# Optimization experiments

Hardware: AMD Instinct MI355X
Metric: run time of the kernel (lower is better)

Reference implementation:

```python
import jax, jax.numpy as jnp
import numpy as np
from jax import lax

B, N, H, W, C = 8, 1024, 256, 256, 256
HID = 512
RATES = (1, 3, 9, 9, 3, 1)


def setup_inputs() -> dict:
    key = jax.random.key(0)
    ks = jax.random.split(key, 16)
    # vertices are (row, col) float coordinates inside the feature map
    vertices = jax.random.uniform(ks[0], (B, N, 2), jnp.float32) * jnp.array([H - 1, W - 1], jnp.float32)
    features = jax.random.normal(ks[1], (B, H, W, C), jnp.float32)
    inp = {"vertices": vertices, "features": features}
    # Conv1D stack params (haiku Conv1D: kernel [K, Cin, Cout], bias [Cout])
    cin = C
    for i in range(6):
        inp[f"w{i}"] = jax.random.normal(ks[2 + 2 * i], (3, cin, HID), jnp.float32) * 0.05
        inp[f"b{i}"] = jax.random.normal(ks[3 + 2 * i], (HID,), jnp.float32) * 0.05
        cin = HID
    # offset head: Conv1D(2, 1, with_bias=False); original zero-init, randomized here
    inp["w_off"] = jax.random.normal(ks[14], (1, HID, 2), jnp.float32) * 0.05
    return inp


def _conv1d(x, w, b, rate):
    # x: [B, N, Cin], w: [K, Cin, Cout] -> SAME-padded dilated conv over vertex axis
    y = lax.conv_general_dilated(x, w, window_strides=(1,), padding="SAME",
                                 rhs_dilation=(rate,),
                                 dimension_numbers=("NWC", "WIO", "NWC"))
    return y if b is None else y + b


def _sample_at_vertices(vertices, features):
    # bilinear interpolation, zero outside (map_coordinates order=1 mode='constant')
    Bb, Hh, Ww, Cc = features.shape
    y, x = vertices[..., 0], vertices[..., 1]  # [B, N]
    y0f, x0f = jnp.floor(y), jnp.floor(x)
    wy1, wx1 = y - y0f, x - x0f
    wy0, wx0 = 1.0 - wy1, 1.0 - wx1
    y0, x0 = y0f.astype(jnp.int32), x0f.astype(jnp.int32)
    flat = features.reshape(Bb, Hh * Ww, Cc)

    def gather(yi, xi, wgt):
        valid = (yi >= 0) & (yi < Hh) & (xi >= 0) & (xi < Ww)
        idx = jnp.clip(yi, 0, Hh - 1) * Ww + jnp.clip(xi, 0, Ww - 1)  # [B, N]
        vals = jnp.take_along_axis(flat, idx[..., None], axis=1)  # [B, N, C]
        return vals * (wgt * valid)[..., None]

    return (gather(y0, x0, wy0 * wx0) + gather(y0, x0 + 1, wy0 * wx1)
            + gather(y0 + 1, x0, wy1 * wx0) + gather(y0 + 1, x0 + 1, wy1 * wx1))


def reference(vertices, features, w0, b0, w1, b1, w2, b2, w3, b3, w4, b4, w5, b5, w_off):
    h = _sample_at_vertices(vertices, features)  # [B, N, C]
    ws = (w0, w1, w2, w3, w4, w5)
    bs = (b0, b1, b2, b3, b4, b5)
    for w, b, r in zip(ws, bs, RATES):
        h = jax.nn.relu(_conv1d(h, w, b, r))
    offsets = _conv1d(h, w_off, None, 1)  # [B, N, 2]
    return vertices + offsets
```

## Files before the change

### kernel.cpp

```cpp
#include <hip/hip_runtime.h>

#define BATCH 8
#define NPTS  1024
#define FH    256
#define FW    256
#define FC    256
#define HID   512
#define PADN  1056
#define HALO  16

typedef __attribute__((ext_vector_type(8))) short short8;
typedef __attribute__((ext_vector_type(16))) float f32x16;
typedef unsigned short ushort_t;
typedef unsigned int uint_t;

__device__ __forceinline__ ushort_t f2bf(float f) {
    uint_t u = __builtin_bit_cast(uint_t, f);
    u += 0x7fffu + ((u >> 16) & 1u);
    return (ushort_t)(u >> 16);
}
__device__ __forceinline__ float bf2f(ushort_t s) {
    uint_t u = ((uint_t)s) << 16;
    return __builtin_bit_cast(float, u);
}

#define GLOAD16(g, l)                                                     \
    __builtin_amdgcn_global_load_lds(                                     \
        (const __attribute__((address_space(1))) void*)(g),               \
        (__attribute__((address_space(3))) void*)(l), 16, 0, 0)

__device__ __forceinline__ short8 gread16(const short* p) {
    short8 r;
    asm volatile("global_load_dwordx4 %0, %1, off" : "=v"(r) : "v"(p));
    return r;
}

__global__ __launch_bounds__(256) void prep_kernel(
    const float* __restrict__ vertices, const float* __restrict__ features,
    const float* __restrict__ w0, const float* __restrict__ w1,
    const float* __restrict__ w2, const float* __restrict__ w3,
    const float* __restrict__ w4, const float* __restrict__ w5,
    ushort_t* __restrict__ wt0, ushort_t* __restrict__ wt1,
    ushort_t* __restrict__ wt2, ushort_t* __restrict__ wt3,
    ushort_t* __restrict__ wt4, ushort_t* __restrict__ wt5,
    ushort_t* __restrict__ XpA, ushort_t* __restrict__ XpB,
    ushort_t* __restrict__ XpC)
{
    __shared__ float tile[64][65];
    const int blk = blockIdx.x;
    const int tid = threadIdx.x;

    if (blk < 1280) {
        int i = blk * 256 + tid;
        if (i < 65536) {
            int b = i >> 13, rem = i & 8191;
            int strip = rem >> 12, off = rem & 4095;
            XpA[(size_t)b * (PADN * FC) + (strip ? (PADN - HALO) * FC : 0) + off] = 0;
        }
        int jB = i - 65536;
        if (jB >= 0 && jB < 262144) {
            ushort_t* T = (jB < 131072) ? XpB : XpC;
            int j = jB & 131071;
            int b = j >> 14, rem = j & 16383;
            int strip = rem >> 13, off = rem & 8191;
            T[(size_t)b * (PADN * HID) + (strip ? (PADN - HALO) * HID : 0) + off] = 0;
        }
        return;
    }

    if (blk < 2336) {
        int j = blk - 1280;
        const float* w; ushort_t* wt; int CIN, kk0, co0;
        if (j < 96) {
            w = w0; wt = wt0; CIN = FC;
            kk0 = (j % 12) * 64; co0 = (j / 12) * 64;
        } else {
            int j2 = j - 96;
            int layer = j2 / 192, jj = j2 % 192;
            const float* ws[5]  = {w1, w2, w3, w4, w5};
            ushort_t*   wts[5]  = {wt1, wt2, wt3, wt4, wt5};
            w = ws[layer]; wt = wts[layer]; CIN = HID;
            kk0 = (jj % 24) * 64; co0 = (jj / 24) * 64;
        }
        int tap = kk0 / CIN, ci0 = kk0 - tap * CIN;
        int SL  = (3 * CIN) >> 4;
#pragma unroll 4
        for (int it = 0; it < 16; ++it) {
            int r = it * 4 + (tid >> 6);
            tile[r][tid & 63] = w[((size_t)tap * CIN + ci0 + r) * HID + co0 + (tid & 63)];
        }
        __syncthreads();
        int gl  = tid >> 7;
        int r2  = tid & 127;
        int l   = r2 >> 1;
        int j0  = (r2 & 1) * 4;
        int gco = (co0 >> 5) + gl;
        int kb  = ((l >> 5) << 3);
        int cl  = gl * 32 + (l & 31);
#pragma unroll
        for (int si = 0; si < 4; ++si) {
            int s = (kk0 >> 4) + si;
            ushort4 v;
            v.x = f2bf(tile[si * 16 + kb + j0 + 0][cl]);
            v.y = f2bf(tile[si * 16 + kb + j0 + 1][cl]);
            v.z = f2bf(tile[si * 16 + kb + j0 + 2][cl]);
            v.w = f2bf(tile[si * 16 + kb + j0 + 3][cl]);
            *(ushort4*)(wt + ((((size_t)gco * SL) + s) << 9) + l * 8 + j0) = v;
        }
        return;
    }

    {
        int p = (blk - 2336) * 4 + (tid >> 6);
        int b = p >> 10;
        int n = p & 1023;
        int t = tid & 63;

        float y = vertices[2 * p + 0];
        float x = vertices[2 * p + 1];
        float y0f = floorf(y), x0f = floorf(x);
        float wy1 = y - y0f, wx1 = x - x0f;
        float wy0 = 1.f - wy1, wx0 = 1.f - wx1;
        int y0 = (int)y0f, x0 = (int)x0f;

        float4 acc = make_float4(0.f, 0.f, 0.f, 0.f);
        const float4* fbase = (const float4*)features + (size_t)b * FH * FW * (FC / 4);

#define CORNER(yi, xi, wgt) {                                                  \
        int yy = (yi), xx = (xi);                                              \
        float wv = ((yy >= 0) && (yy < FH) && (xx >= 0) && (xx < FW)) ? (wgt) : 0.f; \
        int yc = yy < 0 ? 0 : (yy > FH - 1 ? FH - 1 : yy);                     \
        int xc = xx < 0 ? 0 : (xx > FW - 1 ? FW - 1 : xx);                     \
        float4 v = fbase[((size_t)yc * FW + xc) * (FC / 4) + t];               \
        acc.x += v.x * wv; acc.y += v.y * wv; acc.z += v.z * wv; acc.w += v.w * wv; }

        CORNER(y0,     x0,     wy0 * wx0);
        CORNER(y0,     x0 + 1, wy0 * wx1);
        CORNER(y0 + 1, x0,     wy1 * wx0);
        CORNER(y0 + 1, x0 + 1, wy1 * wx1);
#undef CORNER

        ushort4 o;
        o.x = f2bf(acc.x); o.y = f2bf(acc.y); o.z = f2bf(acc.z); o.w = f2bf(acc.w);
        *(ushort4*)(XpA + ((size_t)b * PADN + HALO + n) * FC + 4 * t) = o;
    }
}

template <int CIN>
__global__ __launch_bounds__(512, 2) void conv_mfma(
    const ushort_t* __restrict__ Xp,
    const ushort_t* __restrict__ Wf,
    const float* __restrict__ bias,
    ushort_t* __restrict__ Yp,
    int rate)
{
    constexpr int NC  = CIN / 64;
    constexpr int SL3 = CIN / 16;
    constexpr int SL  = 3 * SL3;
    __shared__ short lds[2][18432];

    const int tid  = threadIdx.x;
    const int wid  = tid >> 6;
    const int lane = tid & 63;
    const int wm   = wid >> 2;
    const int wn   = (wid >> 1) & 1;
    const int wk   = wid & 1;

    const int h  = blockIdx.x;
    const int bm = (h & 7) * 4 + (h >> 6);
    const int bn = (h >> 3) & 7;
    const int batch = bm >> 2;
    const int n0    = (bm & 3) * 256;
    const int co0   = bn * 64;

    const short* Xbase = (const short*)Xp + ((size_t)batch * PADN + n0) * CIN;
    const short* Wb = (const short*)Wf
                    + (((size_t)(bn * 2 + wn) * SL) << 9) + lane * 8;

    auto stageA = [&](int buf, int c) {
        const short* Ag = Xbase + c * 64;
        short* ldsA = &lds[buf][0];
#pragma unroll
        for (int it = 0; it < 4; ++it) {
            int slot = it * 512 + wid * 64 + lane;
            int row  = slot >> 3;
            int chnk = (slot & 7) ^ (row & 7);
            GLOAD16(Ag + (size_t)row * CIN + chnk * 8,
                    ldsA + (size_t)(it * 512 + wid * 64) * 8);
        }
        if (wid < 4) {
            int slot = 2048 + wid * 64 + lane;
            int row  = slot >> 3;
            int chnk = (slot & 7) ^ (row & 7);
            GLOAD16(Ag + (size_t)row * CIN + chnk * 8,
                    ldsA + (size_t)(2048 + wid * 64) * 8);
        }
    };
    auto loadB = [&](short8* dst, int c) {
#pragma unroll
        for (int t = 0; t < 3; ++t)
#pragma unroll
            for (int ksh = 0; ksh < 2; ++ksh)
                dst[t * 2 + ksh] =
                    gread16(Wb + ((size_t)(t * SL3 + c * 4 + wk * 2 + ksh) << 9));
    };

    f32x16 acc[4];
    const int rowA0 = wm * 128 + (lane & 31);
    const int coB   = wn * 32 + (lane & 31);
    {
        float bv = (wk == 0) ? bias[co0 + coB] : 0.f;
#pragma unroll
        for (int i = 0; i < 4; ++i)
#pragma unroll
            for (int r = 0; r < 16; ++r) acc[i][r] = bv;
    }

    short8 B0[6], B1[6];
    stageA(0, 0);
    __builtin_amdgcn_sched_barrier(0);
    loadB(B0, 0);
    __builtin_amdgcn_sched_barrier(0);
    asm volatile("s_waitcnt vmcnt(6)" ::: "memory");
    __builtin_amdgcn_s_barrier();
    __builtin_amdgcn_sched_barrier(0);

    int cur = 0;
    auto kstep = [&](int c, short8* Bcur, short8* Bnxt) {
        if (c + 1 < NC) stageA(cur ^ 1, c + 1);
        __builtin_amdgcn_sched_barrier(0);

        if (c + 1 < NC) asm volatile("s_waitcnt vmcnt(4)" ::: "memory");
        else            asm volatile("s_waitcnt vmcnt(0)" ::: "memory");
        __builtin_amdgcn_sched_barrier(0);

        const short* As = &lds[cur][0];
        __builtin_amdgcn_s_setprio(1);
#pragma unroll
        for (int t = 0; t < 3; ++t) {
            const int shift = 16 + (t - 1) * rate;
#pragma unroll
            for (int ksh = 0; ksh < 2; ++ksh) {
                int ch = (wk * 2 + ksh) * 2 + (lane >> 5);
#pragma unroll
                for (int i = 0; i < 4; ++i) {
                    int rr = rowA0 + i * 32 + shift;
                    short8 av = *(const short8*)(As + rr * 64 + ((ch ^ (rr & 7)) << 3));
                    acc[i] = __builtin_amdgcn_mfma_f32_32x32x16_bf16(
                        av, Bcur[t * 2 + ksh], acc[i], 0, 0, 0);
                }
            }
        }
        __builtin_amdgcn_s_setprio(0);
        __builtin_amdgcn_sched_barrier(0);

        if (c + 1 < NC) {
            loadB(Bnxt, c + 1);
            __builtin_amdgcn_sched_barrier(0);
            asm volatile("s_waitcnt vmcnt(6)" ::: "memory");
        }
        __builtin_amdgcn_s_barrier();
        cur ^= 1;
    };

    for (int c = 0; c < NC; c += 2) {
        kstep(c,     B0, B1);
        kstep(c + 1, B1, B0);
    }

    float* pf = (float*)&lds[0][0];
    const int pair = wm * 2 + wn;
    if (wk == 1) {
#pragma unroll
        for (int i = 0; i < 4; ++i)
#pragma unroll
            for (int r = 0; r < 16; ++r)
                pf[pair * 4096 + (i * 16 + r) * 64 + lane] = acc[i][r];
    }
    __syncthreads();
    if (wk == 0) {
        ushort_t* Yb = Yp + ((size_t)batch * PADN + HALO + n0) * HID + co0;
#pragma unroll
        for (int i = 0; i < 4; ++i) {
#pragma unroll
            for (int r = 0; r < 16; ++r) {
                int rrow = wm * 128 + i * 32 + (r & 3) + 8 * (r >> 2) + 4 * (lane >> 5);
                float v = acc[i][r] + pf[pair * 4096 + (i * 16 + r) * 64 + lane];
                v = v > 0.f ? v : 0.f;
                Yb[(size_t)rrow * HID + coB] = f2bf(v);
            }
        }
    }
}

__global__ __launch_bounds__(64) void head_kernel(
    const ushort_t* __restrict__ h, const float* __restrict__ w_off,
    const float* __restrict__ vertices, float* __restrict__ out)
{
    int p = blockIdx.x;
    int b = p >> 10, n = p & 1023;
    int t = threadIdx.x;
    const ushort_t* hr = h + ((size_t)b * PADN + HALO + n) * HID + t * 8;

    uint4 raw = *(const uint4*)hr;
    ushort_t hv[8];
    hv[0] = raw.x & 0xffff; hv[1] = raw.x >> 16;
    hv[2] = raw.y & 0xffff; hv[3] = raw.y >> 16;
    hv[4] = raw.z & 0xffff; hv[5] = raw.z >> 16;
    hv[6] = raw.w & 0xffff; hv[7] = raw.w >> 16;

    float s0 = 0.f, s1 = 0.f;
#pragma unroll
    for (int k = 0; k < 8; ++k) {
        float x = bf2f(hv[k]);
        s0 += x * w_off[(t * 8 + k) * 2 + 0];
        s1 += x * w_off[(t * 8 + k) * 2 + 1];
    }
#pragma unroll
    for (int off = 32; off >= 1; off >>= 1) {
        s0 += __shfl_down(s0, off);
        s1 += __shfl_down(s1, off);
    }
    if (t == 0) {
        out[2 * p + 0] = vertices[2 * p + 0] + s0;
        out[2 * p + 1] = vertices[2 * p + 1] + s1;
    }
}

extern "C" void kernel_launch(void* const* d_in, const int* in_sizes, int n_in,
                              void* d_out, int out_size, void* d_ws, size_t ws_size,
                              hipStream_t stream)
{
    (void)in_sizes; (void)n_in; (void)out_size; (void)ws_size;

    const float* vertices = (const float*)d_in[0];
    const float* features = (const float*)d_in[1];
    const float* w[6]  = {(const float*)d_in[2], (const float*)d_in[4],
                          (const float*)d_in[6], (const float*)d_in[8],
                          (const float*)d_in[10], (const float*)d_in[12]};
    const float* bb[6] = {(const float*)d_in[3], (const float*)d_in[5],
                          (const float*)d_in[7], (const float*)d_in[9],
                          (const float*)d_in[11], (const float*)d_in[13]};
    const float* w_off = (const float*)d_in[14];
    float* out = (float*)d_out;

    char* p = (char*)d_ws;
    ushort_t* wt[6];
    wt[0] = (ushort_t*)p; p += (size_t)HID * (3 * FC) * 2;
    for (int i = 1; i < 6; ++i) { wt[i] = (ushort_t*)p; p += (size_t)HID * (3 * HID) * 2; }
    ushort_t* XpA = (ushort_t*)p; p += (size_t)BATCH * PADN * FC  * 2;
    ushort_t* XpB = (ushort_t*)p; p += (size_t)BATCH * PADN * HID * 2;
    ushort_t* XpC = (ushort_t*)p;

    prep_kernel<<<4384, 256, 0, stream>>>(
        vertices, features, w[0], w[1], w[2], w[3], w[4], w[5],
        wt[0], wt[1], wt[2], wt[3], wt[4], wt[5], XpA, XpB, XpC);

    static const int rates[6] = {1, 3, 9, 9, 3, 1};
    conv_mfma<FC><<<256, 512, 0, stream>>>(XpA, wt[0], bb[0], XpB, rates[0]);
    ushort_t* src = XpB;
    ushort_t* dst = XpC;
    for (int i = 1; i < 6; ++i) {
        conv_mfma<HID><<<256, 512, 0, stream>>>(src, wt[i], bb[i], dst, rates[i]);
        ushort_t* tmp = src; src = dst; dst = tmp;
    }

    head_kernel<<<BATCH * NPTS, 64, 0, stream>>>(src, w_off, vertices, out);
}
```

Measured before the change: 117.2 us.

## Fuse offset head into last conv and reshape warp split to 4-way K

The final conv layer now computes the 2-channel offset projection directly from its accumulators, using shuffle reductions and atomicAdd into an output that the prep kernel pre-fills with the vertices. This removes the separate head kernel and the store and reload of the last hidden activation. At the same time the warp layout changes: each wave covers both 32-column halves and the K dimension is split four ways instead of two. This doubles the accumulator registers per wave and needs a three-round LDS reduction with extra barriers. The float atomics make the summation order nondeterministic, and the higher register use may hurt occupancy.

```diff
diff --git a/kernel.cpp b/kernel.cpp
--- a/kernel.cpp
+++ b/kernel.cpp
@@ -44,7 +44,7 @@
     ushort_t* __restrict__ wt2, ushort_t* __restrict__ wt3,
     ushort_t* __restrict__ wt4, ushort_t* __restrict__ wt5,
     ushort_t* __restrict__ XpA, ushort_t* __restrict__ XpB,
-    ushort_t* __restrict__ XpC)
+    ushort_t* __restrict__ XpC, float* __restrict__ out)
 {
     __shared__ float tile[64][65];
     const int blk = blockIdx.x;
@@ -110,7 +110,7 @@
         return;
     }
 
-    {
+    if (blk < 4384) {
         int p = (blk - 2336) * 4 + (tid >> 6);
         int b = p >> 10;
         int n = p & 1023;
@@ -143,16 +143,24 @@
         ushort4 o;
         o.x = f2bf(acc.x); o.y = f2bf(acc.y); o.z = f2bf(acc.z); o.w = f2bf(acc.w);
         *(ushort4*)(XpA + ((size_t)b * PADN + HALO + n) * FC + 4 * t) = o;
-    }
-}
-
-template <int CIN>
+        return;
+    }
+
+    {
+        int i = (blk - 4384) * 256 + tid;
+        out[i] = vertices[i];
+    }
+}
+
+template <int CIN, bool HEAD>
 __global__ __launch_bounds__(512, 2) void conv_mfma(
     const ushort_t* __restrict__ Xp,
     const ushort_t* __restrict__ Wf,
     const float* __restrict__ bias,
     ushort_t* __restrict__ Yp,
-    int rate)
+    int rate,
+    const float* __restrict__ w_off,
+    float* __restrict__ out)
 {
     constexpr int NC  = CIN / 64;
     constexpr int SL3 = CIN / 16;
@@ -163,8 +171,7 @@
     const int wid  = tid >> 6;
     const int lane = tid & 63;
     const int wm   = wid >> 2;
-    const int wn   = (wid >> 1) & 1;
-    const int wk   = wid & 1;
+    const int wk   = wid & 3;
 
     const int h  = blockIdx.x;
     const int bm = (h & 7) * 4 + (h >> 6);
@@ -174,8 +181,7 @@
     const int co0   = bn * 64;
 
     const short* Xbase = (const short*)Xp + ((size_t)batch * PADN + n0) * CIN;
-    const short* Wb = (const short*)Wf
-                    + (((size_t)(bn * 2 + wn) * SL) << 9) + lane * 8;
+    const short* Wbase = (const short*)Wf + lane * 8;
 
     auto stageA = [&](int buf, int c) {
         const short* Ag = Xbase + c * 64;
@@ -200,20 +206,22 @@
 #pragma unroll
         for (int t = 0; t < 3; ++t)
 #pragma unroll
-            for (int ksh = 0; ksh < 2; ++ksh)
-                dst[t * 2 + ksh] =
-                    gread16(Wb + ((size_t)(t * SL3 + c * 4 + wk * 2 + ksh) << 9));
+            for (int j = 0; j < 2; ++j) {
+                size_t gco = (size_t)(bn * 2 + j);
+                size_t sl  = (size_t)(t * SL3 + c * 4 + wk);
+                dst[t * 2 + j] = gread16(Wbase + ((gco * SL + sl) << 9));
+            }
     };
 
-    f32x16 acc[4];
+    f32x16 acc[4][2];
     const int rowA0 = wm * 128 + (lane & 31);
-    const int coB   = wn * 32 + (lane & 31);
     {
-        float bv = (wk == 0) ? bias[co0 + coB] : 0.f;
+        float bv0 = (wk == 0) ? bias[co0 + (lane & 31)] : 0.f;
+        float bv1 = (wk == 0) ? bias[co0 + 32 + (lane & 31)] : 0.f;
 #pragma unroll
         for (int i = 0; i < 4; ++i)
 #pragma unroll
-            for (int r = 0; r < 16; ++r) acc[i][r] = bv;
+            for (int r = 0; r < 16; ++r) { acc[i][0][r] = bv0; acc[i][1][r] = bv1; }
     }
 
     short8 B0[6], B1[6];
@@ -235,20 +243,19 @@
         __builtin_amdgcn_sched_barrier(0);
 
         const short* As = &lds[cur][0];
+        const int ch = wk * 2 + (lane >> 5);
         __builtin_amdgcn_s_setprio(1);
 #pragma unroll
         for (int t = 0; t < 3; ++t) {
             const int shift = 16 + (t - 1) * rate;
 #pragma unroll
-            for (int ksh = 0; ksh < 2; ++ksh) {
-                int ch = (wk * 2 + ksh) * 2 + (lane >> 5);
-#pragma unroll
-                for (int i = 0; i < 4; ++i) {
-                    int rr = rowA0 + i * 32 + shift;
-                    short8 av = *(const short8*)(As + rr * 64 + ((ch ^ (rr & 7)) << 3));
-                    acc[i] = __builtin_amdgcn_mfma_f32_32x32x16_bf16(
-                        av, Bcur[t * 2 + ksh], acc[i], 0, 0, 0);
-                }
+            for (int i = 0; i < 4; ++i) {
+                int rr = rowA0 + i * 32 + shift;
+                short8 av = *(const short8*)(As + rr * 64 + ((ch ^ (rr & 7)) << 3));
+                acc[i][0] = __builtin_amdgcn_mfma_f32_32x32x16_bf16(
+                    av, Bcur[t * 2 + 0], acc[i][0], 0, 0, 0);
+                acc[i][1] = __builtin_amdgcn_mfma_f32_32x32x16_bf16(
+                    av, Bcur[t * 2 + 1], acc[i][1], 0, 0, 0);
             }
         }
         __builtin_amdgcn_s_setprio(0);
@@ -269,61 +276,74 @@
     }
 
     float* pf = (float*)&lds[0][0];
-    const int pair = wm * 2 + wn;
-    if (wk == 1) {
-#pragma unroll
-        for (int i = 0; i < 4; ++i)
-#pragma unroll
-            for (int r = 0; r < 16; ++r)
-                pf[pair * 4096 + (i * 16 + r) * 64 + lane] = acc[i][r];
-    }
-    __syncthreads();
+#pragma unroll
+    for (int p = 1; p < 4; ++p) {
+        if (wk == p) {
+#pragma unroll
+            for (int i = 0; i < 4; ++i)
+#pragma unroll
+                for (int j = 0; j < 2; ++j)
+#pragma unroll
+                    for (int r = 0; r < 16; ++r)
+                        pf[wm * 8192 + ((i * 2 + j) * 16 + r) * 64 + lane] = acc[i][j][r];
+        }
+        __syncthreads();
+        if (wk == 0) {
+#pragma unroll
+            for (int i = 0; i < 4; ++i)
+#pragma unroll
+                for (int j = 0; j < 2; ++j)
+#pragma unroll
+                    for (int r = 0; r < 16; ++r)
+                        acc[i][j][r] += pf[wm * 8192 + ((i * 2 + j) * 16 + r) * 64 + lane];
+        }
+        __syncthreads();
+    }
+
     if (wk == 0) {
-        ushort_t* Yb = Yp + ((size_t)batch * PADN + HALO + n0) * HID + co0;
-#pragma unroll
-        for (int i = 0; i < 4; ++i) {
-#pragma unroll
-            for (int r = 0; r < 16; ++r) {
-                int rrow = wm * 128 + i * 32 + (r & 3) + 8 * (r >> 2) + 4 * (lane >> 5);
-                float v = acc[i][r] + pf[pair * 4096 + (i * 16 + r) * 64 + lane];
-                v = v > 0.f ? v : 0.f;
-                Yb[(size_t)rrow * HID + coB] = f2bf(v);
+        if (!HEAD) {
+            ushort_t* Yb = Yp + ((size_t)batch * PADN + HALO + n0) * HID + co0;
+#pragma unroll
+            for (int i = 0; i < 4; ++i) {
+#pragma unroll
+                for (int r = 0; r < 16; ++r) {
+                    int rrow = wm * 128 + i * 32 + (r & 3) + 8 * (r >> 2) + 4 * (lane >> 5);
+#pragma unroll
+                    for (int j = 0; j < 2; ++j) {
+                        float v = acc[i][j][r];
+                        v = v > 0.f ? v : 0.f;
+                        Yb[(size_t)rrow * HID + j * 32 + (lane & 31)] = f2bf(v);
+                    }
+                }
             }
-        }
-    }
-}
-
-__global__ __launch_bounds__(64) void head_kernel(
-    const ushort_t* __restrict__ h, const float* __restrict__ w_off,
-    const float* __restrict__ vertices, float* __restrict__ out)
-{
-    int p = blockIdx.x;
-    int b = p >> 10, n = p & 1023;
-    int t = threadIdx.x;
-    const ushort_t* hr = h + ((size_t)b * PADN + HALO + n) * HID + t * 8;
-
-    uint4 raw = *(const uint4*)hr;
-    ushort_t hv[8];
-    hv[0] = raw.x & 0xffff; hv[1] = raw.x >> 16;
-    hv[2] = raw.y & 0xffff; hv[3] = raw.y >> 16;
-    hv[4] = raw.z & 0xffff; hv[5] = raw.z >> 16;
-    hv[6] = raw.w & 0xffff; hv[7] = raw.w >> 16;
-
-    float s0 = 0.f, s1 = 0.f;
-#pragma unroll
-    for (int k = 0; k < 8; ++k) {
-        float x = bf2f(hv[k]);
-        s0 += x * w_off[(t * 8 + k) * 2 + 0];
-        s1 += x * w_off[(t * 8 + k) * 2 + 1];
-    }
-#pragma unroll
-    for (int off = 32; off >= 1; off >>= 1) {
-        s0 += __shfl_down(s0, off);
-        s1 += __shfl_down(s1, off);
-    }
-    if (t == 0) {
-        out[2 * p + 0] = vertices[2 * p + 0] + s0;
-        out[2 * p + 1] = vertices[2 * p + 1] + s1;
+        } else {
+            const int col = lane & 31;
+            float w00 = w_off[(co0 + col) * 2 + 0];
+            float w01 = w_off[(co0 + col) * 2 + 1];
+            float w10 = w_off[(co0 + 32 + col) * 2 + 0];
+            float w11 = w_off[(co0 + 32 + col) * 2 + 1];
+#pragma unroll
+            for (int i = 0; i < 4; ++i) {
+#pragma unroll
+                for (int r = 0; r < 16; ++r) {
+                    float v0 = acc[i][0][r]; v0 = v0 > 0.f ? v0 : 0.f;
+                    float v1 = acc[i][1][r]; v1 = v1 > 0.f ? v1 : 0.f;
+                    float s0 = v0 * w00 + v1 * w10;
+                    float s1 = v0 * w01 + v1 * w11;
+#pragma unroll
+                    for (int m = 16; m >= 1; m >>= 1) {
+                        s0 += __shfl_xor(s0, m);
+                        s1 += __shfl_xor(s1, m);
+                    }
+                    if (col == 0) {
+                        int row = n0 + wm * 128 + i * 32 + (r & 3) + 8 * (r >> 2) + 4 * (lane >> 5);
+                        float* op = out + 2 * ((size_t)batch * NPTS + row);
+                        atomicAdd(op + 0, s0);
+                        atomicAdd(op + 1, s1);
+                    }
+                }
+            }
+        }
     }
 }
 
@@ -352,18 +372,20 @@
     ushort_t* XpB = (ushort_t*)p; p += (size_t)BATCH * PADN * HID * 2;
     ushort_t* XpC = (ushort_t*)p;
 
-    prep_kernel<<<4384, 256, 0, stream>>>(
+    prep_kernel<<<4448, 256, 0, stream>>>(
         vertices, features, w[0], w[1], w[2], w[3], w[4], w[5],
-        wt[0], wt[1], wt[2], wt[3], wt[4], wt[5], XpA, XpB, XpC);
+        wt[0], wt[1], wt[2], wt[3], wt[4], wt[5], XpA, XpB, XpC, out);
 
     static const int rates[6] = {1, 3, 9, 9, 3, 1};
-    conv_mfma<FC><<<256, 512, 0, stream>>>(XpA, wt[0], bb[0], XpB, rates[0]);
+    conv_mfma<FC, false><<<256, 512, 0, stream>>>(
+        XpA, wt[0], bb[0], XpB, rates[0], nullptr, nullptr);
     ushort_t* src = XpB;
     ushort_t* dst = XpC;
-    for (int i = 1; i < 6; ++i) {
-        conv_mfma<HID><<<256, 512, 0, stream>>>(src, wt[i], bb[i], dst, rates[i]);
+    for (int i = 1; i < 5; ++i) {
+        conv_mfma<HID, false><<<256, 512, 0, stream>>>(
+            src, wt[i], bb[i], dst, rates[i], nullptr, nullptr);
         ushort_t* tmp = src; src = dst; dst = tmp;
     }
-
-    head_kernel<<<BATCH * NPTS, 64, 0, stream>>>(src, w_off, vertices, out);
-}
+    conv_mfma<HID, true><<<256, 512, 0, stream>>>(
+        src, wt[5], bb[5], dst, rates[5], w_off, out);
+}
```

Result: slower. 142.4 us (+21.5%).

## Fuse six conv layer launches into one cooperative kernel with grid syncs

Applied to the files above, without the earlier changes.

Replaces six separate conv kernel launches with a single cooperative kernel that runs all layers in sequence, separated by grid-wide barriers. It keeps a fallback to per-layer launches if the cooperative launch fails. The goal is to remove per-launch overhead and the drain/ramp gaps between layers. In exchange it adds grid.sync cost, depends on all 256 blocks being co-resident, and sharing one kernel body may change register allocation.

```diff
diff --git a/kernel.cpp b/kernel.cpp
--- a/kernel.cpp
+++ b/kernel.cpp
@@ -1,4 +1,7 @@
 #include <hip/hip_runtime.h>
+#include <hip/hip_cooperative_groups.h>
+
+namespace cg = cooperative_groups;
 
 #define BATCH 8
 #define NPTS  1024
@@ -147,17 +150,14 @@
 }
 
 template <int CIN>
-__global__ __launch_bounds__(512, 2) void conv_mfma(
-    const ushort_t* __restrict__ Xp,
-    const ushort_t* __restrict__ Wf,
-    const float* __restrict__ bias,
-    ushort_t* __restrict__ Yp,
-    int rate)
+__device__ __forceinline__ void conv_layer(
+    const ushort_t* __restrict__ Xp, const ushort_t* __restrict__ Wf,
+    const float* __restrict__ bias, ushort_t* __restrict__ Yp, int rate,
+    short (*lds)[18432])
 {
     constexpr int NC  = CIN / 64;
     constexpr int SL3 = CIN / 16;
     constexpr int SL  = 3 * SL3;
-    __shared__ short lds[2][18432];
 
     const int tid  = threadIdx.x;
     const int wid  = tid >> 6;
@@ -291,6 +291,37 @@
             }
         }
     }
+    __syncthreads();
+}
+
+struct ConvArgs {
+    const ushort_t* XpA; ushort_t* XpB; ushort_t* XpC;
+    const ushort_t* wt0; const ushort_t* wt1; const ushort_t* wt2;
+    const ushort_t* wt3; const ushort_t* wt4; const ushort_t* wt5;
+    const float* b0; const float* b1; const float* b2;
+    const float* b3; const float* b4; const float* b5;
+};
+
+__global__ __launch_bounds__(512, 2) void conv_fused(ConvArgs a)
+{
+    __shared__ short lds[2][18432];
+    cg::grid_group grid = cg::this_grid();
+
+    conv_layer<FC >(a.XpA, a.wt0, a.b0, a.XpB, 1, lds); grid.sync();
+    conv_layer<HID>(a.XpB, a.wt1, a.b1, a.XpC, 3, lds); grid.sync();
+    conv_layer<HID>(a.XpC, a.wt2, a.b2, a.XpB, 9, lds); grid.sync();
+    conv_layer<HID>(a.XpB, a.wt3, a.b3, a.XpC, 9, lds); grid.sync();
+    conv_layer<HID>(a.XpC, a.wt4, a.b4, a.XpB, 3, lds); grid.sync();
+    conv_layer<HID>(a.XpB, a.wt5, a.b5, a.XpC, 1, lds);
+}
+
+template <int CIN>
+__global__ __launch_bounds__(512, 2) void conv_single(
+    const ushort_t* __restrict__ Xp, const ushort_t* __restrict__ Wf,
+    const float* __restrict__ bias, ushort_t* __restrict__ Yp, int rate)
+{
+    __shared__ short lds[2][18432];
+    conv_layer<CIN>(Xp, Wf, bias, Yp, rate, lds);
 }
 
 __global__ __launch_bounds__(64) void head_kernel(
@@ -356,14 +387,24 @@
         vertices, features, w[0], w[1], w[2], w[3], w[4], w[5],
         wt[0], wt[1], wt[2], wt[3], wt[4], wt[5], XpA, XpB, XpC);
 
-    static const int rates[6] = {1, 3, 9, 9, 3, 1};
-    conv_mfma<FC><<<256, 512, 0, stream>>>(XpA, wt[0], bb[0], XpB, rates[0]);
-    ushort_t* src = XpB;
-    ushort_t* dst = XpC;
-    for (int i = 1; i < 6; ++i) {
-        conv_mfma<HID><<<256, 512, 0, stream>>>(src, wt[i], bb[i], dst, rates[i]);
-        ushort_t* tmp = src; src = dst; dst = tmp;
-    }
-
-    head_kernel<<<BATCH * NPTS, 64, 0, stream>>>(src, w_off, vertices, out);
-}
+    ConvArgs ca = { XpA, XpB, XpC,
+                    wt[0], wt[1], wt[2], wt[3], wt[4], wt[5],
+                    bb[0], bb[1], bb[2], bb[3], bb[4], bb[5] };
+    void* args[] = { &ca };
+    hipError_t ce = hipLaunchCooperativeKernel(
+        reinterpret_cast<void*>(conv_fused), dim3(256), dim3(512),
+        args, 0, stream);
+    if (ce != hipSuccess) {
+        (void)hipGetLastError();
+        static const int rates[6] = {1, 3, 9, 9, 3, 1};
+        conv_single<FC><<<256, 512, 0, stream>>>(XpA, wt[0], bb[0], XpB, rates[0]);
+        ushort_t* src = XpB;
+        ushort_t* dst = XpC;
+        for (int i = 1; i < 6; ++i) {
+            conv_single<HID><<<256, 512, 0, stream>>>(src, wt[i], bb[i], dst, rates[i]);
+            ushort_t* tmp = src; src = dst; dst = tmp;
+        }
+    }
+
+    head_kernel<<<BATCH * NPTS, 64, 0, stream>>>(XpC, w_off, vertices, out);
+}
```

Result: slower. 270.1 us (+130.4%).
